# Kernel optimization log

Hardware: AMD Instinct MI355X
Metric: run time of the kernel (lower is better)

Reference implementation:

```python
import jax, jax.numpy as jnp
import numpy as np

D = 1024
H = 8
HD = D // H
SCALE = HD ** -0.5


def setup_inputs() -> dict:
    key = jax.random.key(0)
    ks = jax.random.split(key, 12)
    s = 0.02
    return {
        "x": jax.random.normal(ks[0], (4, 2048, D), dtype=jnp.float32),
        "attn_mask": jax.random.randint(ks[1], (2048, 2048), 0, 2, dtype=jnp.int32),
        "qkv_w": jax.random.normal(ks[2], (3 * D, D), dtype=jnp.float32) * s,
        "qkv_b": jnp.zeros((3 * D,), dtype=jnp.float32),
        "q_w": jax.random.normal(ks[3], (D, D), dtype=jnp.float32) * s,
        "q_b": jnp.zeros((D,), dtype=jnp.float32),
        "k_w": jax.random.normal(ks[4], (D, D), dtype=jnp.float32) * s,
        "k_b": jnp.zeros((D,), dtype=jnp.float32),
        "v_w": jax.random.normal(ks[5], (D, D), dtype=jnp.float32) * s,
        "v_b": jnp.zeros((D,), dtype=jnp.float32),
        "out_w": jax.random.normal(ks[6], (D, D), dtype=jnp.float32) * s,
        "out_b": jnp.zeros((D,), dtype=jnp.float32),
    }


def reference(x, attn_mask, qkv_w, qkv_b, q_w, q_b, k_w, k_b, v_w, v_b, out_w, out_b):
    B, S, _ = x.shape
    qkv = x @ qkv_w.T + qkv_b
    q, k, v = jnp.split(qkv, 3, axis=-1)
    # per-stream multi-head projections, then split heads: [B,H,S,HD]
    def heads(t, w, b):
        return (t @ w.T + b).reshape(B, S, H, HD).transpose(0, 2, 1, 3)
    q = heads(q, q_w, q_b)
    k = heads(k, k_w, k_b)
    v = heads(v, v_w, v_b)
    # scaled dot-product attention with masked softmax
    scores = jnp.einsum("bhqd,bhkd->bhqk", q, k) * SCALE
    scores = jnp.where(attn_mask == 1, -jnp.inf, scores)
    attn = jax.nn.softmax(scores, axis=-1)
    o = jnp.einsum("bhqk,bhkd->bhqd", attn, v)
    o = o.transpose(0, 2, 1, 3).reshape(B, S, D)
    return o @ out_w.T + out_b
```

## Files before the change

kernel.cpp:

```cpp
#include <hip/hip_runtime.h>
#include <stdint.h>

typedef unsigned short u16;
typedef unsigned int u32;
typedef unsigned long long u64;
using f32x4 = __attribute__((ext_vector_type(4))) float;
using f32x16 = __attribute__((ext_vector_type(16))) float;
using s16x8 = __attribute__((ext_vector_type(8))) short;
using u16x4 = __attribute__((ext_vector_type(4))) unsigned short;
using u32x4 = __attribute__((ext_vector_type(4))) u32;

static constexpr float kQScale = (float)(0.08838834764831845 * 1.4426950408889634);

__device__ __forceinline__ u16 f2bf(float f) {
  uint32_t u = __float_as_uint(f);
  u += 0x7fffu + ((u >> 16) & 1u);
  return (u16)(u >> 16);
}

__device__ __forceinline__ float fexp2(float x) {
#if __has_builtin(__builtin_amdgcn_exp2f)
  return __builtin_amdgcn_exp2f(x);
#else
  return exp2f(x);
#endif
}

__device__ __forceinline__ u32 cvtpk(float lo, float hi) {
  u32 r;
  asm("v_cvt_pk_bf16_f32 %0, %1, %2" : "=v"(r) : "v"(lo), "v"(hi));
  return r;
}

__device__ __forceinline__ void mfma16(f32x4& d, s16x8 a, s16x8 b) {
  asm volatile("v_mfma_f32_16x16x32_bf16 %0, %1, %2, %0" : "+v"(d) : "v"(a), "v"(b));
}
__device__ __forceinline__ void mfma32(f32x16& d, s16x8 a, s16x8 b) {
  asm volatile("v_mfma_f32_32x32x16_bf16 %0, %1, %2, %0" : "+v"(d) : "v"(a), "v"(b));
}
__device__ __forceinline__ f32x16 mfma32_z(s16x8 a, s16x8 b) {
  f32x16 d;
  asm volatile("v_mfma_f32_32x32x16_bf16 %0, %1, %2, 0" : "=&v"(d) : "v"(a), "v"(b));
  return d;
}

__device__ __forceinline__ void g2lds16(const void* g, void* l) {
  __builtin_amdgcn_global_load_lds(
      (__attribute__((address_space(1))) void*)(uintptr_t)g,
      (__attribute__((address_space(3))) void*)(uint32_t)(uintptr_t)l, 16, 0, 0);
}

#define BAR() asm volatile("s_barrier" ::: "memory")

__global__ __launch_bounds__(256) void prep(const float* __restrict__ x, u16* __restrict__ xb,
                                            const float* __restrict__ qw, const float* __restrict__ kw,
                                            const float* __restrict__ vw, const float* __restrict__ ow,
                                            u16* __restrict__ wb4,
                                            const float* __restrict__ qkvw, u16* __restrict__ qkvwT,
                                            const float* __restrict__ qkvb, const float* __restrict__ qb,
                                            const float* __restrict__ kb, const float* __restrict__ vb,
                                            float* __restrict__ cb3,
                                            const int* __restrict__ am, u64* __restrict__ pm) {
  __shared__ u16 tile[32][33];
  const int bid = blockIdx.x, tid = threadIdx.x;
  if (bid < 8192) {
    int i = (bid * 256 + tid) * 4;
    f32x4 v = *(const f32x4*)(x + i);
    u16x4 o = {f2bf(v.x), f2bf(v.y), f2bf(v.z), f2bf(v.w)};
    *(u16x4*)(xb + i) = o;
  } else if (bid < 12288) {
    int idx = bid - 8192;
    int z = idx >> 10;
    const float* in = z == 0 ? qw : z == 1 ? kw : z == 2 ? vw : ow;
    int i = ((idx & 1023) * 256 + tid) * 4;
    f32x4 v = *(const f32x4*)(in + i);
    u16x4 o = {f2bf(v.x), f2bf(v.y), f2bf(v.z), f2bf(v.w)};
    *(u16x4*)(wb4 + (size_t)z * 1048576 + i) = o;
  } else if (bid < 15360) {
    int idx = bid - 12288;
    int bx = idx & 31, by = idx >> 5;
    int tx = tid & 31, ty = tid >> 5;
#pragma unroll
    for (int k = 0; k < 4; ++k)
      tile[ty + k * 8][tx] = f2bf(qkvw[(size_t)(by * 32 + ty + k * 8) * 1024 + bx * 32 + tx]);
    __syncthreads();
#pragma unroll
    for (int k = 0; k < 4; ++k)
      qkvwT[(size_t)(bx * 32 + ty + k * 8) * 3072 + by * 32 + tx] = tile[tx][ty + k * 8];
  } else if (bid < 16128) {
    int idx = bid - 15360;
    int z = idx >> 8;
    const float* w = z == 0 ? qw : (z == 1 ? kw : vw);
    const float* ba = z == 0 ? qb : (z == 1 ? kb : vb);
    const float* bi = qkvb + z * 1024;
    int o = (idx & 255) * 4 + (tid >> 6);
    int lane = tid & 63;
    float s = 0.f;
    for (int m = lane; m < 1024; m += 64) s += w[o * 1024 + m] * bi[m];
#pragma unroll
    for (int d = 1; d < 64; d <<= 1) s += __shfl_xor(s, d);
    if (lane == 0) {
      float fin = s + ba[o];
      if (z == 0) fin *= kQScale;
      cb3[z * 1024 + o] = fin;
    }
  } else {
    int row = bid - 16128;
    int wv = tid >> 6, lane = tid & 63;
#pragma unroll
    for (int i = 0; i < 8; ++i) {
      int word = wv * 8 + i;
      u64 b = __ballot(am[(size_t)row * 2048 + word * 64 + lane] == 0);
      if (lane == 0) pm[(size_t)row * 32 + word] = b;
    }
  }
}

template <typename OUT_T, bool BIAS_PER_ROW>
__global__ __launch_bounds__(256, 2) void gemm_nt(const u16* __restrict__ A, int lda, long bsA,
                                                  const u16* __restrict__ B, int ldb, long bsB,
                                                  OUT_T* __restrict__ C, int ldc, long bsC,
                                                  const float* __restrict__ bias, long bsBias,
                                                  int NtilesN, int K, float scale_z0) {
  __shared__ __align__(16) u16 As[128 * 64];
  __shared__ __align__(16) u16 Bs[128 * 64];
  const int z = blockIdx.z;
  const float sc = (z == 0) ? scale_z0 : 1.f;
  A += (size_t)z * bsA; B += (size_t)z * bsB; C += (size_t)z * bsC;
  if (bias) bias += (size_t)z * bsBias;
  const int tm = blockIdx.x / NtilesN, tn = blockIdx.x % NtilesN;
  const int tid = threadIdx.x, lane = tid & 63, w = tid >> 6;
  const int wm = w >> 1, wn = w & 1;
  const int q = lane & 15, g = lane >> 4;
  f32x4 acc[4][4] = {};

  const u16* Ab = A + (size_t)(tm * 128 + (tid >> 3)) * lda + ((tid & 7) << 3);
  const u16* Bb = B + (size_t)(tn * 128 + (tid >> 3)) * ldb + ((tid & 7) << 3);
  char* AsW = (char*)As + (w << 10);
  char* BsW = (char*)Bs + (w << 10);

  for (int k0 = 0; k0 < K; k0 += 64) {
#pragma unroll
    for (int it = 0; it < 4; ++it) {
      g2lds16(Ab + (size_t)(it * 32) * lda + k0, AsW + it * 4096);
      g2lds16(Bb + (size_t)(it * 32) * ldb + k0, BsW + it * 4096);
    }
    __syncthreads();
#pragma unroll
    for (int kk = 0; kk < 2; ++kk) {
      s16x8 af[4], bf[4];
#pragma unroll
      for (int i = 0; i < 4; ++i)
        af[i] = *(const s16x8*)((const char*)As + (wm * 64 + i * 16 + q) * 128 + kk * 64 + g * 16);
#pragma unroll
      for (int i = 0; i < 4; ++i)
        bf[i] = *(const s16x8*)((const char*)Bs + (wn * 64 + i * 16 + q) * 128 + kk * 64 + g * 16);
#pragma unroll
      for (int mf = 0; mf < 4; ++mf)
#pragma unroll
        for (int nf = 0; nf < 4; ++nf) mfma16(acc[mf][nf], af[mf], bf[nf]);
    }
    __syncthreads();
  }
  asm volatile("s_nop 7\n\ts_nop 7");
#pragma unroll
  for (int mf = 0; mf < 4; ++mf)
#pragma unroll
    for (int nf = 0; nf < 4; ++nf) {
      const int row = tm * 128 + wm * 64 + mf * 16 + g * 4;
      const int col = tn * 128 + wn * 64 + nf * 16 + q;
      float bc = (!BIAS_PER_ROW && bias) ? bias[col] : 0.f;
#pragma unroll
      for (int r = 0; r < 4; ++r) {
        float v = acc[mf][nf][r] * sc;
        if (bias) v += BIAS_PER_ROW ? bias[row + r] : bc;
        if constexpr (sizeof(OUT_T) == 2)
          C[(size_t)(row + r) * ldc + col] = (OUT_T)f2bf(v);
        else
          C[(size_t)(row + r) * ldc + col] = (OUT_T)v;
      }
    }
}

__global__ __launch_bounds__(512, 4) void gemm_qk(const u16* __restrict__ A,
                                                  const u16* __restrict__ B,
                                                  const float* __restrict__ bias,
                                                  u16* __restrict__ C) {
  __shared__ __align__(16) u16 As[256 * 64];
  __shared__ __align__(16) u16 Bs[128 * 64];
  const int bid = blockIdx.x;
  const int wgid = (bid & 7) * 64 + (bid >> 3);
  const int tm = wgid >> 4, tn = wgid & 15;
  const int tid = threadIdx.x, lane = tid & 63, w = tid >> 6;
  const int wm = w >> 1, wn = w & 1;
  const int q = lane & 15, g = lane >> 4, qk = q & 7;
  f32x4 acc[4][4] = {};

  const int srow = tid >> 3, sch = tid & 7;
  const int gcol = (sch ^ (srow & 7)) << 3;
  const u16* Abase = A + (size_t)(tm * 256 + srow) * 1024 + gcol;
  const u16* Bbase = B + (size_t)(tn * 128 + srow) * 1024 + gcol;
  char* AsW = (char*)As + (w << 10);
  char* BsW = (char*)Bs + (w << 10);

  for (int k0 = 0; k0 < 1024; k0 += 64) {
#pragma unroll
    for (int it = 0; it < 4; ++it)
      g2lds16(Abase + (size_t)(it * 64) * 1024 + k0, AsW + it * 8192);
#pragma unroll
    for (int it = 0; it < 2; ++it)
      g2lds16(Bbase + (size_t)(it * 64) * 1024 + k0, BsW + it * 8192);
    __syncthreads();
#pragma unroll
    for (int kk = 0; kk < 2; ++kk) {
      s16x8 af[4], bf[4];
#pragma unroll
      for (int i = 0; i < 4; ++i)
        af[i] = *(const s16x8*)((const char*)As + (wm * 64 + i * 16 + q) * 128 +
                                ((((kk << 2) + g) ^ qk) << 4));
#pragma unroll
      for (int i = 0; i < 4; ++i)
        bf[i] = *(const s16x8*)((const char*)Bs + (wn * 64 + i * 16 + q) * 128 +
                                ((((kk << 2) + g) ^ qk) << 4));
      __builtin_amdgcn_s_setprio(1);
#pragma unroll
      for (int mf = 0; mf < 4; ++mf)
#pragma unroll
        for (int nf = 0; nf < 4; ++nf) mfma16(acc[mf][nf], af[mf], bf[nf]);
      __builtin_amdgcn_s_setprio(0);
    }
    __syncthreads();
  }
  asm volatile("s_nop 7\n\ts_nop 7");
#pragma unroll
  for (int mf = 0; mf < 4; ++mf) {
    const int row = tm * 256 + wm * 64 + mf * 16 + g * 4;
#pragma unroll
    for (int nf = 0; nf < 4; ++nf) {
      const int col = tn * 128 + wn * 64 + nf * 16 + q;
      const float bc = bias[col];
#pragma unroll
      for (int r = 0; r < 4; ++r)
        C[(size_t)(row + r) * 2048 + col] = f2bf(acc[mf][nf][r] + bc);
    }
  }
}

__global__ __launch_bounds__(256, 2) void attn_fwd(const u16* __restrict__ Qb, const u16* __restrict__ Kb,
                                                   int ldq, const u16* __restrict__ Vt,
                                                   const u64* __restrict__ pmask,
                                                   u16* __restrict__ Ob) {
  __shared__ __align__(16) char K_lds[2][16384];
  __shared__ __align__(16) char V_lds[3][16384];
  const int n = blockIdx.x;
  const int slot = n >> 3;
  const int grp = (n & 7) * 4 + (slot >> 4);
  const int qt = slot & 15;
  const int h = grp & 7, b = grp >> 3;
  const int tid = threadIdx.x, w = tid >> 6, lane = tid & 63;
  const int ql = lane & 31;
  const int hi = lane >> 5;
  const int q0 = qt * 128;

  s16x8 qf[8];
  const u16* qrow = Qb + (size_t)(b * 2048 + q0 + w * 32 + ql) * ldq + h * 128 + 8 * hi;
#pragma unroll
  for (int kd = 0; kd < 8; ++kd) qf[kd] = *(const s16x8*)(qrow + 16 * kd);

  u32x4 ov = {0x3F803F80u, 0x3F803F80u, 0x3F803F80u, 0x3F803F80u};
  const s16x8 ones = __builtin_bit_cast(s16x8, ov);

  f32x16 oacc[4] = {};
  f32x16 lacc = {};

  const int ksr = tid >> 4, ksc = tid & 15;
  const int vsr = tid >> 3, vsc = tid & 7;
  const int sw = ql & 15;
  const u64* pmrow = pmask + (size_t)(q0 + w * 32 + ql) * 32;

  auto stageK = [&](int buf, int s2) {
    const int kv0 = s2 * 64;
    char* kb = K_lds[buf] + (w << 10);
#pragma unroll
    for (int it = 0; it < 4; ++it) {
      int kr = it * 16 + ksr;
      g2lds16(Kb + (size_t)(b * 2048 + kv0 + kr) * ldq + h * 128 + ((ksc ^ (kr & 15)) << 3),
              kb + it * 4096);
    }
  };
  auto stageV = [&](int buf, int s2) {
    const int kv0 = s2 * 64;
    char* vb = V_lds[buf] + (w << 10);
#pragma unroll
    for (int it = 0; it < 4; ++it) {
      int vr = it * 32 + vsr;
      g2lds16(Vt + (size_t)(h * 128 + vr) * 8192 + b * 2048 + kv0 + ((vsc ^ (vr & 7)) << 3),
              vb + it * 4096);
    }
  };
  auto qk = [&](f32x16& d0, f32x16& d1, int kbuf) {
    const char* Kc = K_lds[kbuf];
#pragma unroll
    for (int kd = 0; kd < 8; ++kd) {
      int c = (2 * kd + hi) ^ sw;
      s16x8 kf0 = *(const s16x8*)(Kc + ql * 256 + (c << 4));
      s16x8 kf1 = *(const s16x8*)(Kc + (32 + ql) * 256 + (c << 4));
      if (kd == 0) { d0 = mfma32_z(kf0, qf[0]); d1 = mfma32_z(kf1, qf[0]); }
      else         { mfma32(d0, kf0, qf[kd]);   mfma32(d1, kf1, qf[kd]); }
    }
  };

  auto body = [&](f32x16& c0, f32x16& c1, f32x16& n0, f32x16& n1, int s, int vbR, int vbW) {
    u64 pw = pmrow[s];
    const int sc2 = (s + 2 < 32) ? s + 2 : 31;
    stageK(s & 1, sc2);
    stageV(vbW, sc2);
    if (s + 1 < 32) qk(n0, n1, (s + 1) & 1);
    const char* Vc = V_lds[vbR];
    s16x8 pa[2];
#pragma unroll
    for (int half = 0; half < 2; ++half) {
      u32 halfm = (u32)(pw >> (32 * half + 4 * hi));
      u32 Wp[4][2];
#pragma unroll
      for (int t = 0; t < 4; ++t) {
        float e[4];
#pragma unroll
        for (int j = 0; j < 4; ++j) {
          float ev = fexp2(half == 0 ? c0[4 * t + j] : c1[4 * t + j]);
          int km;
          asm("v_bfe_i32 %0, %1, %2, 1" : "=v"(km) : "v"(halfm), "n"(8 * t + j));
          e[j] = __uint_as_float(__float_as_uint(ev) & (u32)km);
        }
        Wp[t][0] = cvtpk(e[0], e[1]);
        Wp[t][1] = cvtpk(e[2], e[3]);
      }
#pragma unroll
      for (int kq = 0; kq < 2; ++kq) {
        u32 s0 = hi ? Wp[2 * kq][0] : Wp[2 * kq + 1][0];
        u32 s1 = hi ? Wp[2 * kq][1] : Wp[2 * kq + 1][1];
        u32 r0 = (u32)__shfl_xor((int)s0, 32);
        u32 r1 = (u32)__shfl_xor((int)s1, 32);
        u32 o0 = hi ? Wp[2 * kq + 1][0] : Wp[2 * kq][0];
        u32 o1 = hi ? Wp[2 * kq + 1][1] : Wp[2 * kq][1];
        u32x4 wv;
        wv.x = hi ? r0 : o0;
        wv.y = hi ? r1 : o1;
        wv.z = hi ? o0 : r0;
        wv.w = hi ? o1 : r1;
        pa[kq] = __builtin_bit_cast(s16x8, wv);
      }
      asm volatile("s_nop 3");
      __builtin_amdgcn_s_setprio(1);
#pragma unroll
      for (int kq = 0; kq < 2; ++kq) {
        const int ks = 2 * half + kq;
#pragma unroll
        for (int dt = 0; dt < 4; ++dt) {
          int vrow = dt * 32 + ql;
          s16x8 vf = *(const s16x8*)(Vc + vrow * 128 + (((2 * ks + hi) ^ (vrow & 7)) << 4));
          mfma32(oacc[dt], pa[kq], vf);
        }
        mfma32(lacc, pa[kq], ones);
      }
      __builtin_amdgcn_s_setprio(0);
    }
    asm volatile("s_waitcnt vmcnt(4)" ::: "memory");
    BAR();
  };

  stageK(0, 0); stageV(0, 0); stageK(1, 1); stageV(1, 1);
  asm volatile("s_waitcnt vmcnt(4)" ::: "memory");
  BAR();
  f32x16 sA0, sA1, sB0, sB1;
  qk(sA0, sA1, 0);
  BAR();

  int vb = 0;
  for (int s2 = 0; s2 < 16; ++s2) {
    const int s = 2 * s2;
    const int vb1 = (vb + 1 == 3) ? 0 : vb + 1;
    const int vb2 = (vb + 2 >= 3) ? vb - 1 : vb + 2;
    body(sA0, sA1, sB0, sB1, s, vb, vb2);
    body(sB0, sB1, sA0, sA1, s + 1, vb1, vb);
    vb = vb2;
  }

  asm volatile("s_nop 7\n\ts_nop 7");
#pragma unroll
  for (int dt = 0; dt < 4; ++dt)
#pragma unroll
    for (int reg = 0; reg < 16; ++reg) {
      int qr = (reg & 3) + 8 * (reg >> 2) + 4 * hi;
      size_t trow = (size_t)(b * 2048 + q0 + w * 32 + qr);
      Ob[trow * 1024 + h * 128 + dt * 32 + ql] = f2bf(oacc[dt][reg] / lacc[reg]);
    }
}

extern "C" void kernel_launch(void* const* d_in, const int* in_sizes, int n_in,
                              void* d_out, int out_size, void* d_ws, size_t ws_size,
                              hipStream_t stream) {
  (void)in_sizes; (void)n_in; (void)out_size; (void)ws_size;
  const float* x    = (const float*)d_in[0];
  const int*   am   = (const int*)d_in[1];
  const float* qkvw = (const float*)d_in[2];
  const float* qkvb = (const float*)d_in[3];
  const float* qw   = (const float*)d_in[4];
  const float* qb   = (const float*)d_in[5];
  const float* kw   = (const float*)d_in[6];
  const float* kb   = (const float*)d_in[7];
  const float* vw   = (const float*)d_in[8];
  const float* vb   = (const float*)d_in[9];
  const float* ow   = (const float*)d_in[10];
  const float* ob   = (const float*)d_in[11];

  char* p = (char*)d_ws;
  auto take = [&](size_t n) { char* r = p; p += (n + 255) & ~(size_t)255; return r; };
  u16* xb    = (u16*)take(8192ull * 1024 * 2);
  u16* qkvwT = (u16*)take(1024ull * 3072 * 2);
  u16* wb4   = (u16*)take(4ull * 1048576 * 2);
  u16* comb3 = (u16*)take(3ull * 1048576 * 2);
  float* cb3 = (float*)take(3ull * 1024 * 4);
  u16* QK2   = (u16*)take(8192ull * 2048 * 2);
  u16* V2t   = (u16*)take(8192ull * 1024 * 2);
  u64* pm    = (u64*)take(2048ull * 32 * 8);
  u16* Obuf  = xb;

  prep<<<18176, 256, 0, stream>>>(x, xb, qw, kw, vw, ow, wb4, qkvw, qkvwT,
                                  qkvb, qb, kb, vb, cb3, am, pm);
  gemm_nt<u16, false><<<dim3(64, 1, 3), 256, 0, stream>>>(
      wb4, 1024, 1048576, qkvwT, 3072, 1024, comb3, 1024, 1048576, nullptr, 0, 8, 1024, kQScale);
  gemm_qk<<<512, 512, 0, stream>>>(xb, comb3, cb3, QK2);
  gemm_nt<u16, true><<<dim3(512, 1, 1), 256, 0, stream>>>(
      comb3 + 2 * 1048576, 1024, 0, xb, 1024, 0, V2t, 8192, 0, cb3 + 2048, 0, 64, 1024, 1.f);
  attn_fwd<<<512, 256, 0, stream>>>(QK2, QK2 + 1024, 2048, V2t, pm, Obuf);
  gemm_nt<float, false><<<dim3(512, 1, 1), 256, 0, stream>>>(
      Obuf, 1024, 0, wb4 + 3 * 1048576, 1024, 0, (float*)d_out, 1024, 0, ob, 0, 8, 1024, 1.f);
}
```

Measured before the change: 239.3 us.

## Split attention KV range across two wave groups with LDS reduction

```diff
diff --git a/kernel.cpp b/kernel.cpp
--- a/kernel.cpp
+++ b/kernel.cpp
@@ -246,155 +246,174 @@
   }
 }
 
-__global__ __launch_bounds__(256, 2) void attn_fwd(const u16* __restrict__ Qb, const u16* __restrict__ Kb,
+__global__ __launch_bounds__(512, 4) void attn_fwd(const u16* __restrict__ Qb, const u16* __restrict__ Kb,
                                                    int ldq, const u16* __restrict__ Vt,
                                                    const u64* __restrict__ pmask,
                                                    u16* __restrict__ Ob) {
-  __shared__ __align__(16) char K_lds[2][16384];
-  __shared__ __align__(16) char V_lds[3][16384];
+  __shared__ __align__(16) char smem[81920];
   const int n = blockIdx.x;
   const int slot = n >> 3;
   const int grp = (n & 7) * 4 + (slot >> 4);
   const int qt = slot & 15;
   const int h = grp & 7, b = grp >> 3;
   const int tid = threadIdx.x, w = tid >> 6, lane = tid & 63;
-  const int ql = lane & 31;
-  const int hi = lane >> 5;
+  const int t = w >> 2, ws = w & 3;
+  const int ql = lane & 31, hi = lane >> 5;
   const int q0 = qt * 128;
+  const int kvbase = b * 2048 + t * 1024;
 
   s16x8 qf[8];
-  const u16* qrow = Qb + (size_t)(b * 2048 + q0 + w * 32 + ql) * ldq + h * 128 + 8 * hi;
+  const u16* qrow = Qb + (size_t)(b * 2048 + q0 + ws * 32 + ql) * ldq + h * 128 + 8 * hi;
 #pragma unroll
   for (int kd = 0; kd < 8; ++kd) qf[kd] = *(const s16x8*)(qrow + 16 * kd);
 
-  u32x4 ov = {0x3F803F80u, 0x3F803F80u, 0x3F803F80u, 0x3F803F80u};
-  const s16x8 ones = __builtin_bit_cast(s16x8, ov);
-
   f32x16 oacc[4] = {};
-  f32x16 lacc = {};
-
-  const int ksr = tid >> 4, ksc = tid & 15;
-  const int vsr = tid >> 3, vsc = tid & 7;
+  float lp = 0.f;
+
+  const int st = tid & 255;
+  const int ksr = st >> 4, ksc = st & 15;
+  const int vsr = st >> 2, vsc = st & 3;
   const int sw = ql & 15;
-  const u64* pmrow = pmask + (size_t)(q0 + w * 32 + ql) * 32;
-
-  auto stageK = [&](int buf, int s2) {
-    const int kv0 = s2 * 64;
-    char* kb = K_lds[buf] + (w << 10);
-#pragma unroll
-    for (int it = 0; it < 4; ++it) {
+  const u64* pmrow = pmask + (size_t)(q0 + ws * 32 + ql) * 32 + t * 16;
+
+  auto stageK = [&](int buf, int si) {
+    const int kv0 = si * 32;
+    char* kb = smem + (t * 2 + buf) * 8192 + (ws << 10);
+#pragma unroll
+    for (int it = 0; it < 2; ++it) {
       int kr = it * 16 + ksr;
-      g2lds16(Kb + (size_t)(b * 2048 + kv0 + kr) * ldq + h * 128 + ((ksc ^ (kr & 15)) << 3),
+      g2lds16(Kb + (size_t)(kvbase + kv0 + kr) * ldq + h * 128 + ((ksc ^ (kr & 15)) << 3),
               kb + it * 4096);
     }
   };
-  auto stageV = [&](int buf, int s2) {
-    const int kv0 = s2 * 64;
-    char* vb = V_lds[buf] + (w << 10);
-#pragma unroll
-    for (int it = 0; it < 4; ++it) {
-      int vr = it * 32 + vsr;
-      g2lds16(Vt + (size_t)(h * 128 + vr) * 8192 + b * 2048 + kv0 + ((vsc ^ (vr & 7)) << 3),
-              vb + it * 4096);
+  auto stageV = [&](int buf, int si) {
+    const int kv0 = si * 32;
+    char* vbp = smem + 32768 + (t * 3 + buf) * 8192 + (ws << 10);
+#pragma unroll
+    for (int it = 0; it < 2; ++it) {
+      int vr = it * 64 + vsr;
+      g2lds16(Vt + (size_t)(h * 128 + vr) * 8192 + kvbase + kv0 + ((vsc ^ (vr & 3)) << 3),
+              vbp + it * 4096);
     }
   };
-  auto qk = [&](f32x16& d0, f32x16& d1, int kbuf) {
-    const char* Kc = K_lds[kbuf];
+  auto qk = [&](f32x16& d0, int kbuf) {
+    const char* Kc = smem + (t * 2 + kbuf) * 8192;
 #pragma unroll
     for (int kd = 0; kd < 8; ++kd) {
       int c = (2 * kd + hi) ^ sw;
-      s16x8 kf0 = *(const s16x8*)(Kc + ql * 256 + (c << 4));
-      s16x8 kf1 = *(const s16x8*)(Kc + (32 + ql) * 256 + (c << 4));
-      if (kd == 0) { d0 = mfma32_z(kf0, qf[0]); d1 = mfma32_z(kf1, qf[0]); }
-      else         { mfma32(d0, kf0, qf[kd]);   mfma32(d1, kf1, qf[kd]); }
+      s16x8 kf = *(const s16x8*)(Kc + ql * 256 + (c << 4));
+      if (kd == 0) d0 = mfma32_z(kf, qf[0]);
+      else         mfma32(d0, kf, qf[kd]);
     }
   };
 
-  auto body = [&](f32x16& c0, f32x16& c1, f32x16& n0, f32x16& n1, int s, int vbR, int vbW) {
-    u64 pw = pmrow[s];
+  stageV(0, 0); stageK(0, 0); stageV(1, 1); stageK(1, 1);
+  asm volatile("s_waitcnt vmcnt(0)" ::: "memory");
+  BAR();
+
+  int vb = 0;
+  for (int s = 0; s < 32; ++s) {
+    const int vbW = (vb + 2 >= 3) ? vb - 1 : vb + 2;
     const int sc2 = (s + 2 < 32) ? s + 2 : 31;
+    stageV(vbW, sc2);
+    f32x16 sacc;
+    __builtin_amdgcn_s_setprio(1);
+    qk(sacc, s & 1);
+    __builtin_amdgcn_s_setprio(0);
+    BAR();
     stageK(s & 1, sc2);
-    stageV(vbW, sc2);
-    if (s + 1 < 32) qk(n0, n1, (s + 1) & 1);
-    const char* Vc = V_lds[vbR];
+
+    u64 mw = pmrow[s >> 1];
+    u32 pw = (u32)(mw >> ((s & 1) * 32));
+    u32 halfm = pw >> (4 * hi);
+    asm volatile("s_nop 7\n\ts_nop 7");
+    u32 Wp[4][2];
+#pragma unroll
+    for (int t2 = 0; t2 < 4; ++t2) {
+      float e[4];
+#pragma unroll
+      for (int j = 0; j < 4; ++j) {
+        float ev = fexp2(sacc[4 * t2 + j]);
+        int km;
+        asm("v_bfe_i32 %0, %1, %2, 1" : "=v"(km) : "v"(halfm), "n"(8 * t2 + j));
+        e[j] = __uint_as_float(__float_as_uint(ev) & (u32)km);
+      }
+      lp += (e[0] + e[1]) + (e[2] + e[3]);
+      Wp[t2][0] = cvtpk(e[0], e[1]);
+      Wp[t2][1] = cvtpk(e[2], e[3]);
+    }
     s16x8 pa[2];
 #pragma unroll
-    for (int half = 0; half < 2; ++half) {
-      u32 halfm = (u32)(pw >> (32 * half + 4 * hi));
-      u32 Wp[4][2];
-#pragma unroll
-      for (int t = 0; t < 4; ++t) {
-        float e[4];
-#pragma unroll
-        for (int j = 0; j < 4; ++j) {
-          float ev = fexp2(half == 0 ? c0[4 * t + j] : c1[4 * t + j]);
-          int km;
-          asm("v_bfe_i32 %0, %1, %2, 1" : "=v"(km) : "v"(halfm), "n"(8 * t + j));
-          e[j] = __uint_as_float(__float_as_uint(ev) & (u32)km);
-        }
-        Wp[t][0] = cvtpk(e[0], e[1]);
-        Wp[t][1] = cvtpk(e[2], e[3]);
+    for (int kq = 0; kq < 2; ++kq) {
+      u32 s0 = hi ? Wp[2 * kq][0] : Wp[2 * kq + 1][0];
+      u32 s1 = hi ? Wp[2 * kq][1] : Wp[2 * kq + 1][1];
+      u32 r0 = (u32)__shfl_xor((int)s0, 32);
+      u32 r1 = (u32)__shfl_xor((int)s1, 32);
+      u32 o0 = hi ? Wp[2 * kq + 1][0] : Wp[2 * kq][0];
+      u32 o1 = hi ? Wp[2 * kq + 1][1] : Wp[2 * kq][1];
+      u32x4 wv;
+      wv.x = hi ? r0 : o0;
+      wv.y = hi ? r1 : o1;
+      wv.z = hi ? o0 : r0;
+      wv.w = hi ? o1 : r1;
+      pa[kq] = __builtin_bit_cast(s16x8, wv);
+    }
+    asm volatile("s_nop 3");
+    const char* Vc = smem + 32768 + (t * 3 + vb) * 8192;
+    __builtin_amdgcn_s_setprio(1);
+#pragma unroll
+    for (int kq = 0; kq < 2; ++kq)
+#pragma unroll
+      for (int dt = 0; dt < 4; ++dt) {
+        int vrow = dt * 32 + ql;
+        s16x8 vf = *(const s16x8*)(Vc + vrow * 64 + (((2 * kq + hi) ^ (vrow & 3)) << 4));
+        mfma32(oacc[dt], pa[kq], vf);
       }
-#pragma unroll
-      for (int kq = 0; kq < 2; ++kq) {
-        u32 s0 = hi ? Wp[2 * kq][0] : Wp[2 * kq + 1][0];
-        u32 s1 = hi ? Wp[2 * kq][1] : Wp[2 * kq + 1][1];
-        u32 r0 = (u32)__shfl_xor((int)s0, 32);
-        u32 r1 = (u32)__shfl_xor((int)s1, 32);
-        u32 o0 = hi ? Wp[2 * kq + 1][0] : Wp[2 * kq][0];
-        u32 o1 = hi ? Wp[2 * kq + 1][1] : Wp[2 * kq][1];
-        u32x4 wv;
-        wv.x = hi ? r0 : o0;
-        wv.y = hi ? r1 : o1;
-        wv.z = hi ? o0 : r0;
-        wv.w = hi ? o1 : r1;
-        pa[kq] = __builtin_bit_cast(s16x8, wv);
-      }
-      asm volatile("s_nop 3");
-      __builtin_amdgcn_s_setprio(1);
-#pragma unroll
-      for (int kq = 0; kq < 2; ++kq) {
-        const int ks = 2 * half + kq;
-#pragma unroll
-        for (int dt = 0; dt < 4; ++dt) {
-          int vrow = dt * 32 + ql;
-          s16x8 vf = *(const s16x8*)(Vc + vrow * 128 + (((2 * ks + hi) ^ (vrow & 7)) << 4));
-          mfma32(oacc[dt], pa[kq], vf);
-        }
-        mfma32(lacc, pa[kq], ones);
-      }
-      __builtin_amdgcn_s_setprio(0);
-    }
-    asm volatile("s_waitcnt vmcnt(4)" ::: "memory");
+    __builtin_amdgcn_s_setprio(0);
+    asm volatile("s_waitcnt vmcnt(2)" ::: "memory");
     BAR();
-  };
-
-  stageK(0, 0); stageV(0, 0); stageK(1, 1); stageV(1, 1);
-  asm volatile("s_waitcnt vmcnt(4)" ::: "memory");
-  BAR();
-  f32x16 sA0, sA1, sB0, sB1;
-  qk(sA0, sA1, 0);
-  BAR();
-
-  int vb = 0;
-  for (int s2 = 0; s2 < 16; ++s2) {
-    const int s = 2 * s2;
-    const int vb1 = (vb + 1 == 3) ? 0 : vb + 1;
-    const int vb2 = (vb + 2 >= 3) ? vb - 1 : vb + 2;
-    body(sA0, sA1, sB0, sB1, s, vb, vb2);
-    body(sB0, sB1, sA0, sA1, s + 1, vb1, vb);
-    vb = vb2;
-  }
-
+    vb = (vb + 1 == 3) ? 0 : vb + 1;
+  }
+
+  asm volatile("s_waitcnt vmcnt(0)" ::: "memory");
+  __syncthreads();
   asm volatile("s_nop 7\n\ts_nop 7");
-#pragma unroll
-  for (int dt = 0; dt < 4; ++dt)
+  lp += __shfl_xor(lp, 32);
+  float* scr = (float*)smem;
+  if (lane < 32) scr[16384 + (t * 4 + ws) * 32 + lane] = lp;
+  if (t == 1) {
+    union { f32x16 v; f32x4 p[4]; } u;
+#pragma unroll
+    for (int dt = 0; dt < 4; ++dt) {
+      u.v = oacc[dt];
+#pragma unroll
+      for (int pc = 0; pc < 4; ++pc)
+        *(f32x4*)(scr + ((dt * 4 + pc) * 256 + ws * 64 + lane) * 4) = u.p[pc];
+    }
+  }
+  __syncthreads();
+  if (t == 0) {
+    float rl[16];
 #pragma unroll
     for (int reg = 0; reg < 16; ++reg) {
       int qr = (reg & 3) + 8 * (reg >> 2) + 4 * hi;
-      size_t trow = (size_t)(b * 2048 + q0 + w * 32 + qr);
-      Ob[trow * 1024 + h * 128 + dt * 32 + ql] = f2bf(oacc[dt][reg] / lacc[reg]);
-    }
+      rl[reg] = 1.f / (scr[16384 + ws * 32 + qr] + scr[16384 + (4 + ws) * 32 + qr]);
+    }
+#pragma unroll
+    for (int dt = 0; dt < 4; ++dt) {
+      union { f32x16 v; f32x4 p[4]; } o2;
+#pragma unroll
+      for (int pc = 0; pc < 4; ++pc)
+        o2.p[pc] = *(const f32x4*)(scr + ((dt * 4 + pc) * 256 + ws * 64 + lane) * 4);
+#pragma unroll
+      for (int reg = 0; reg < 16; ++reg) {
+        int qr = (reg & 3) + 8 * (reg >> 2) + 4 * hi;
+        size_t trow = (size_t)(b * 2048 + q0 + ws * 32 + qr);
+        Ob[trow * 1024 + h * 128 + dt * 32 + ql] =
+            f2bf((oacc[dt][reg] + o2.v[reg]) * rl[reg]);
+      }
+    }
+  }
 }
 
 extern "C" void kernel_launch(void* const* d_in, const int* in_sizes, int n_in,
@@ -433,7 +452,7 @@
   gemm_qk<<<512, 512, 0, stream>>>(xb, comb3, cb3, QK2);
   gemm_nt<u16, true><<<dim3(512, 1, 1), 256, 0, stream>>>(
       comb3 + 2 * 1048576, 1024, 0, xb, 1024, 0, V2t, 8192, 0, cb3 + 2048, 0, 64, 1024, 1.f);
-  attn_fwd<<<512, 256, 0, stream>>>(QK2, QK2 + 1024, 2048, V2t, pm, Obuf);
+  attn_fwd<<<512, 512, 0, stream>>>(QK2, QK2 + 1024, 2048, V2t, pm, Obuf);
   gemm_nt<float, false><<<dim3(512, 1, 1), 256, 0, stream>>>(
       Obuf, 1024, 0, wb4 + 3 * 1048576, 1024, 0, (float*)d_out, 1024, 0, ob, 0, 8, 1024, 1.f);
 }
```

Measured after the change: 350.7 us. 46.5% more time.
